# Kernel tuning notes

Hardware: AMD Instinct MI355X
Metric: run time of the kernel (lower is better)

Reference implementation:

```python
import jax, jax.numpy as jnp
import numpy as np

BLOCK_SIZE = 512


def setup_inputs() -> dict:
    key = jax.random.key(0)
    k1, k2, k3 = jax.random.split(key, 3)
    N, D_IN, NUM_BLOCKS = 8192, 2048, 8
    x = jax.random.normal(k1, (N, D_IN), dtype=jnp.float32)
    # Rademacher +/-1 signs per block
    s_hash = jnp.sign(jax.random.normal(k2, (NUM_BLOCKS, D_IN), dtype=jnp.float32))
    s_hash = jnp.where(s_hash == 0, 1.0, s_hash)
    # hash bucket index in [0, BLOCK_SIZE) per block, per input dim
    i_hash = jax.random.randint(k3, (NUM_BLOCKS, D_IN), 0, BLOCK_SIZE, dtype=jnp.int32)
    return {"x": x, "s_hash": s_hash, "i_hash": i_hash}


def reference(x, s_hash, i_hash):
    # x: [N, d_in]; s_hash: [B, d_in] (+/-1); i_hash: [B, d_in] in [0, block_size)
    N = x.shape[0]
    B = s_hash.shape[0]

    def one_block(s, ih):
        y = x * s  # [N, d_in] sign flip
        # scatter-add columns into block_size buckets (duplicates accumulate)
        return jnp.zeros((N, BLOCK_SIZE), x.dtype).at[:, ih].add(y)

    out = jax.vmap(one_block)(s_hash, i_hash)      # [B, N, block_size]
    out = jnp.moveaxis(out, 0, 1).reshape(N, B * BLOCK_SIZE)  # [N, d_features]
    return out / np.sqrt(B).astype(np.float32)
```

## Files before the change

kernel.cpp:

```cpp
#include <hip/hip_runtime.h>
#include <cstddef>

#define NUM_BLOCKS 8
#define BLK 512
#define D_IN 2048
#define NROWS 8192
#define NBUCKETS (NUM_BLOCKS * BLK)
#define CAP 32
#define ROWS_PER_WG 4
#define THREADS 512
#define SENT 4096

typedef float    v4f __attribute__((ext_vector_type(4)));
typedef unsigned v4u __attribute__((ext_vector_type(4)));

__global__ __launch_bounds__(256) void cs_build_index(
    const int* __restrict__ i_hash, const float* __restrict__ s_hash,
    int* __restrict__ nchunks, int* __restrict__ entries,
    unsigned short* __restrict__ entries16)
{
    const int gid  = blockIdx.x * blockDim.x + threadIdx.x;
    const int wave = gid >> 6;
    const int lane = threadIdx.x & 63;
    if (wave >= NBUCKETS) return;
    const int b = wave >> 9;
    const int k = wave & (BLK - 1);
    const int*   ih = i_hash + b * D_IN;
    const float* sr = s_hash + b * D_IN;
    int* erow = entries + wave * CAP;
    unsigned short* e16 = entries16 + wave * 8;
    int cnt = 0;
    for (int d0 = 0; d0 < D_IN; d0 += 64) {
        const int d = d0 + lane;
        const bool m = (ih[d] == k);
        const unsigned long long mask = __ballot(m);
        if (m) {
            const int pos = cnt + __popcll(mask & ((1ull << lane) - 1ull));
            const int ent = (d << 1) | ((sr[d] < 0.0f) ? 1 : 0);
            if (pos < CAP) erow[pos] = ent;
            if (pos < 8)   e16[pos]  = (unsigned short)ent;
        }
        cnt += (int)__popcll(mask);
    }
    if (cnt > CAP) cnt = CAP;
    int nch = (cnt + 3) >> 2;
    if (nch == 0) nch = 1;
    if (lane >= cnt) {
        if (lane < 8)       e16[lane]  = (unsigned short)SENT;
        if (lane < nch * 4) erow[lane] = SENT;
    }
    if (lane == 0) nchunks[wave] = nch;
}

static __device__ __forceinline__ unsigned bfr(float f) {
    const unsigned u = __float_as_uint(f);
    return (u + 0x7fffu + ((u >> 16) & 1u)) >> 16;
}

__global__ __launch_bounds__(THREADS) void cs_gather(
    const float* __restrict__ x, const int* __restrict__ nchunks,
    const int* __restrict__ entries, const v4u* __restrict__ entries16,
    float* __restrict__ out)
{
    __shared__ uint2 xs2[D_IN + 1];
    const int tid  = threadIdx.x;
    const int row0 = blockIdx.x * ROWS_PER_WG;

    v4u e8[8];
    int nch[8];
#pragma unroll
    for (int g = 0; g < 2; ++g)
#pragma unroll
        for (int q = 0; q < 4; ++q) {
            const int j = 4 * (tid + 512 * g) + q;
            e8[g * 4 + q]  = entries16[j];
            nch[g * 4 + q] = nchunks[j];
        }

    if (tid == 0) xs2[D_IN] = make_uint2(0u, 0u);

    const size_t b0 = (size_t)row0 * D_IN;
#pragma unroll
    for (int i = 0; i < 4; ++i) {
        const int d = tid + i * THREADS;
        uint2 w;
        w.x = bfr(x[b0 + d]) | (bfr(x[b0 + D_IN + d]) << 16);
        w.y = bfr(x[b0 + 2 * D_IN + d]) | (bfr(x[b0 + 3 * D_IN + d]) << 16);
        xs2[d] = w;
    }
    __syncthreads();

    const float scale = 0.35355339059327373f;
#define ASF __uint_as_float

#define PE(e, A)                                                          \
    do {                                                                  \
        const unsigned ue = (unsigned)(e);                                \
        const unsigned sm = (ue & 1u) ? 0x80008000u : 0u;                 \
        const uint2 w = xs2[ue >> 1];                                     \
        const unsigned w0 = w.x ^ sm, w1 = w.y ^ sm;                      \
        A[0] += ASF(w0 << 16); A[1] += ASF(w0 & 0xffff0000u);             \
        A[2] += ASF(w1 << 16); A[3] += ASF(w1 & 0xffff0000u);             \
    } while (0)

#pragma unroll
    for (int g = 0; g < 2; ++g) {
        const int col4 = tid + 512 * g;
        float acc[4][4];
#pragma unroll
        for (int q = 0; q < 4; ++q)
#pragma unroll
            for (int rr = 0; rr < 4; ++rr) acc[q][rr] = 0.0f;

#pragma unroll
        for (int q = 0; q < 4; ++q) {
            const v4u ew = e8[g * 4 + q];
            PE(ew.x & 0xffffu, acc[q]); PE(ew.x >> 16, acc[q]);
            PE(ew.y & 0xffffu, acc[q]); PE(ew.y >> 16, acc[q]);
            PE(ew.z & 0xffffu, acc[q]); PE(ew.z >> 16, acc[q]);
            PE(ew.w & 0xffffu, acc[q]);
            PE(ew.w >> 16, acc[q]);
            const int n = nch[g * 4 + q];
            if (n > 2) {
                const int j = 4 * col4 + q;
                const int4* __restrict__ ep = (const int4*)(entries + j * CAP);
#pragma unroll 1
                for (int c = 2; c < n; ++c) {
                    const int4 cc = ep[c];
                    PE(cc.x, acc[q]); PE(cc.y, acc[q]);
                    PE(cc.z, acc[q]); PE(cc.w, acc[q]);
                }
            }
        }
#pragma unroll
        for (int rr = 0; rr < 4; ++rr) {
            v4f v = { acc[0][rr] * scale, acc[1][rr] * scale,
                      acc[2][rr] * scale, acc[3][rr] * scale };
            __builtin_nontemporal_store(
                v, (v4f*)(out + (size_t)(row0 + rr) * NBUCKETS + 4 * col4));
        }
    }
#undef PE
#undef ASF
}

extern "C" void kernel_launch(void* const* d_in, const int* in_sizes, int n_in,
                              void* d_out, int out_size, void* d_ws, size_t ws_size,
                              hipStream_t stream)
{
    const float* x      = (const float*)d_in[0];
    const float* s_hash = (const float*)d_in[1];
    const int*   i_hash = (const int*)d_in[2];
    float* out = (float*)d_out;

    int* nchunks = (int*)d_ws;
    int* entries = nchunks + NBUCKETS;
    unsigned short* entries16 = (unsigned short*)(entries + NBUCKETS * CAP);

    cs_build_index<<<(NBUCKETS * 64) / 256, 256, 0, stream>>>(
        i_hash, s_hash, nchunks, entries, entries16);
    cs_gather<<<NROWS / ROWS_PER_WG, THREADS, 0, stream>>>(
        x, nchunks, entries, (const v4u*)entries16, out);
}
```

Measured before the change: 56.47 us.

## Process multiple row tiles per workgroup with software-pipelined staging and stores

Each workgroup now loops over four 4-row tiles instead of handling a single tile, so the per-column hash entries and chunk counts loaded into registers are reused across 16 rows. The loop defers the store of the second column group until after the next tile is staged, and uses manual lgkmcnt waits plus raw barriers in place of __syncthreads. This is meant to amortize the index loads and overlap global loads with compute and stores. In exchange it cuts the grid to 512 workgroups and raises register pressure, which the launch bound of 2 waves/EU may force into spills.

```diff
diff --git a/kernel.cpp b/kernel.cpp
--- a/kernel.cpp
+++ b/kernel.cpp
@@ -7,9 +7,11 @@
 #define NROWS 8192
 #define NBUCKETS (NUM_BLOCKS * BLK)
 #define CAP 32
-#define ROWS_PER_WG 4
 #define THREADS 512
 #define SENT 4096
+#define TILES 4
+#define TROWS 4
+#define NWG (NROWS / (TILES * TROWS))
 
 typedef float    v4f __attribute__((ext_vector_type(4)));
 typedef unsigned v4u __attribute__((ext_vector_type(4)));
@@ -57,43 +59,52 @@
     return (u + 0x7fffu + ((u >> 16) & 1u)) >> 16;
 }
 
-__global__ __launch_bounds__(THREADS) void cs_gather(
+__global__ __launch_bounds__(THREADS, 2) void cs_gather(
     const float* __restrict__ x, const int* __restrict__ nchunks,
     const int* __restrict__ entries, const v4u* __restrict__ entries16,
     float* __restrict__ out)
 {
     __shared__ uint2 xs2[D_IN + 1];
-    const int tid  = threadIdx.x;
-    const int row0 = blockIdx.x * ROWS_PER_WG;
+    const int tid      = threadIdx.x;
+    const int row_base = blockIdx.x * (TILES * TROWS);
 
     v4u e8[8];
-    int nch[8];
+    int nch8[8];
 #pragma unroll
     for (int g = 0; g < 2; ++g)
 #pragma unroll
         for (int q = 0; q < 4; ++q) {
             const int j = 4 * (tid + 512 * g) + q;
             e8[g * 4 + q]  = entries16[j];
-            nch[g * 4 + q] = nchunks[j];
+            nch8[g * 4 + q] = nchunks[j];
         }
-
     if (tid == 0) xs2[D_IN] = make_uint2(0u, 0u);
-
-    const size_t b0 = (size_t)row0 * D_IN;
-#pragma unroll
-    for (int i = 0; i < 4; ++i) {
-        const int d = tid + i * THREADS;
-        uint2 w;
-        w.x = bfr(x[b0 + d]) | (bfr(x[b0 + D_IN + d]) << 16);
-        w.y = bfr(x[b0 + 2 * D_IN + d]) | (bfr(x[b0 + 3 * D_IN + d]) << 16);
-        xs2[d] = w;
-    }
-    __syncthreads();
 
     const float scale = 0.35355339059327373f;
 #define ASF __uint_as_float
 
-#define PE(e, A)                                                          \
+#define LGKMBAR() do {                                                    \
+        asm volatile("s_waitcnt lgkmcnt(0)" ::: "memory");                \
+        __builtin_amdgcn_s_barrier();                                     \
+    } while (0)
+
+#define STAGE(t) do {                                                     \
+        const size_t bs = (size_t)(row_base + (t) * TROWS) * D_IN;        \
+        _Pragma("unroll")                                                 \
+        for (int i = 0; i < 4; ++i) {                                     \
+            const int d = tid + i * THREADS;                              \
+            float f0 = x[bs + d];                                         \
+            float f1 = x[bs + D_IN + d];                                  \
+            float f2 = x[bs + 2 * D_IN + d];                              \
+            float f3 = x[bs + 3 * D_IN + d];                              \
+            uint2 w;                                                      \
+            w.x = bfr(f0) | (bfr(f1) << 16);                              \
+            w.y = bfr(f2) | (bfr(f3) << 16);                              \
+            xs2[d] = w;                                                   \
+        }                                                                 \
+    } while (0)
+
+#define PE4(e, A)                                                         \
     do {                                                                  \
         const unsigned ue = (unsigned)(e);                                \
         const unsigned sm = (ue & 1u) ? 0x80008000u : 0u;                 \
@@ -103,44 +114,72 @@
         A[2] += ASF(w1 << 16); A[3] += ASF(w1 & 0xffff0000u);             \
     } while (0)
 
-#pragma unroll
-    for (int g = 0; g < 2; ++g) {
-        const int col4 = tid + 512 * g;
-        float acc[4][4];
-#pragma unroll
-        for (int q = 0; q < 4; ++q)
-#pragma unroll
-            for (int rr = 0; rr < 4; ++rr) acc[q][rr] = 0.0f;
-
-#pragma unroll
-        for (int q = 0; q < 4; ++q) {
-            const v4u ew = e8[g * 4 + q];
-            PE(ew.x & 0xffffu, acc[q]); PE(ew.x >> 16, acc[q]);
-            PE(ew.y & 0xffffu, acc[q]); PE(ew.y >> 16, acc[q]);
-            PE(ew.z & 0xffffu, acc[q]); PE(ew.z >> 16, acc[q]);
-            PE(ew.w & 0xffffu, acc[q]);
-            PE(ew.w >> 16, acc[q]);
-            const int n = nch[g * 4 + q];
-            if (n > 2) {
-                const int j = 4 * col4 + q;
-                const int4* __restrict__ ep = (const int4*)(entries + j * CAP);
+#define COMPG(gb, ACC) do {                                               \
+        _Pragma("unroll")                                                 \
+        for (int q = 0; q < 4; ++q)                                       \
+            _Pragma("unroll")                                             \
+            for (int rr = 0; rr < 4; ++rr) ACC[q][rr] = 0.0f;             \
+        _Pragma("unroll")                                                 \
+        for (int q = 0; q < 4; ++q) {                                     \
+            const v4u ew = e8[(gb) * 4 + q];                              \
+            PE4(ew.x & 0xffffu, ACC[q]); PE4(ew.x >> 16, ACC[q]);         \
+            PE4(ew.y & 0xffffu, ACC[q]); PE4(ew.y >> 16, ACC[q]);         \
+            PE4(ew.z & 0xffffu, ACC[q]); PE4(ew.z >> 16, ACC[q]);         \
+            PE4(ew.w & 0xffffu, ACC[q]);                                  \
+            PE4(ew.w >> 16, ACC[q]);                                      \
+            const int n = nch8[(gb) * 4 + q];                             \
+            if (n > 2) {                                                  \
+                const int j = 4 * (tid + 512 * (gb)) + q;                 \
+                const int4* __restrict__ ep =                             \
+                    (const int4*)(entries + j * CAP);                     \
+                _Pragma("unroll 1")                                       \
+                for (int c = 2; c < n; ++c) {                             \
+                    const int4 cc = ep[c];                                \
+                    PE4(cc.x, ACC[q]); PE4(cc.y, ACC[q]);                 \
+                    PE4(cc.z, ACC[q]); PE4(cc.w, ACC[q]);                 \
+                }                                                         \
+            }                                                             \
+        }                                                                 \
+    } while (0)
+
+#define STOREG(gb, t, ACC) do {                                           \
+        const int c4 = tid + 512 * (gb);                                  \
+        _Pragma("unroll")                                                 \
+        for (int rr = 0; rr < 4; ++rr) {                                  \
+            v4f v = { ACC[0][rr] * scale, ACC[1][rr] * scale,             \
+                      ACC[2][rr] * scale, ACC[3][rr] * scale };           \
+            __builtin_nontemporal_store(                                  \
+                v, (v4f*)(out + (size_t)(row_base + (t) * TROWS + rr) *   \
+                          NBUCKETS + 4 * c4));                            \
+        }                                                                 \
+    } while (0)
+
+    float a0[4][4];
+    float c1[4][4];
+
+    STAGE(0);
+    LGKMBAR();
+    COMPG(0, a0); STOREG(0, 0, a0);
+    COMPG(1, c1);
+    LGKMBAR();
+
 #pragma unroll 1
-                for (int c = 2; c < n; ++c) {
-                    const int4 cc = ep[c];
-                    PE(cc.x, acc[q]); PE(cc.y, acc[q]);
-                    PE(cc.z, acc[q]); PE(cc.w, acc[q]);
-                }
-            }
-        }
-#pragma unroll
-        for (int rr = 0; rr < 4; ++rr) {
-            v4f v = { acc[0][rr] * scale, acc[1][rr] * scale,
-                      acc[2][rr] * scale, acc[3][rr] * scale };
-            __builtin_nontemporal_store(
-                v, (v4f*)(out + (size_t)(row0 + rr) * NBUCKETS + 4 * col4));
-        }
+    for (int t = 1; t < TILES; ++t) {
+        STAGE(t);
+        LGKMBAR();
+        STOREG(1, t - 1, c1);
+        COMPG(0, a0); STOREG(0, t, a0);
+        COMPG(1, c1);
+        LGKMBAR();
     }
-#undef PE
+
+    STOREG(1, TILES - 1, c1);
+
+#undef STOREG
+#undef COMPG
+#undef PE4
+#undef STAGE
+#undef LGKMBAR
 #undef ASF
 }
 
@@ -159,6 +198,6 @@
 
     cs_build_index<<<(NBUCKETS * 64) / 256, 256, 0, stream>>>(
         i_hash, s_hash, nchunks, entries, entries16);
-    cs_gather<<<NROWS / ROWS_PER_WG, THREADS, 0, stream>>>(
+    cs_gather<<<NWG, THREADS, 0, stream>>>(
         x, nchunks, entries, (const v4u*)entries16, out);
 }
```

Result: slower. 68.97 us (+22.1%).
